# Kernel optimization log

Hardware: AMD Instinct MI355X
Metric: run time of the kernel (lower is better)

Reference implementation:

```python
import jax, jax.numpy as jnp
import numpy as np

K = 3          # pred_ks
EMB_SCALE = 1.0


def _unfold(x, k):
    # torch nn.Unfold(kernel=k, padding=(k-1)//2, stride=1), channel-major (C, kh, kw)
    B, C, H, W = x.shape
    p = (k - 1) // 2
    xp = jnp.pad(x, ((0, 0), (0, 0), (p, p), (p, p)))
    pats = jnp.stack([xp[:, :, i:i + H, j:j + W] for i in range(k) for j in range(k)], axis=2)
    return pats.reshape(B, C * k * k, H, W)


def _gs2d_nearest(x, grid):
    # F.grid_sample(mode='nearest', padding_mode='zeros', align_corners=False)
    B, C, H, W = x.shape
    ix = jnp.round((grid[..., 0] + 1.0) * W / 2.0 - 0.5)
    iy = jnp.round((grid[..., 1] + 1.0) * H / 2.0 - 0.5)
    valid = (ix >= 0) & (ix <= W - 1) & (iy >= 0) & (iy <= H - 1)
    ixc = jnp.clip(ix, 0, W - 1).astype(jnp.int32)
    iyc = jnp.clip(iy, 0, H - 1).astype(jnp.int32)

    def samp(img, yy, xx, vv):
        return jnp.where(vv[None], img[:, yy, xx], 0.0)

    return jax.vmap(samp)(x, iyc, ixc, valid)


def _gs3d_trilinear(vol, coords):
    # F.grid_sample 3D, mode='bilinear', padding_mode='zeros', align_corners=False
    # vol [C,D,H,W]; coords [N,3] with (x->W, y->H, z->D)
    C, D, H, W = vol.shape
    x = (coords[:, 0] + 1.0) * W / 2.0 - 0.5
    y = (coords[:, 1] + 1.0) * H / 2.0 - 0.5
    z = (coords[:, 2] + 1.0) * D / 2.0 - 0.5
    x0, y0, z0 = jnp.floor(x), jnp.floor(y), jnp.floor(z)
    vol_f = vol.reshape(C, D * H * W)
    out = jnp.zeros((C, coords.shape[0]), vol.dtype)
    for dz in (0.0, 1.0):
        for dy in (0.0, 1.0):
            for dx in (0.0, 1.0):
                xi, yi, zi = x0 + dx, y0 + dy, z0 + dz
                wgt = (1.0 - jnp.abs(x - xi)) * (1.0 - jnp.abs(y - yi)) * (1.0 - jnp.abs(z - zi))
                valid = (xi >= 0) & (xi <= W - 1) & (yi >= 0) & (yi <= H - 1) & (zi >= 0) & (zi <= D - 1)
                idx = (jnp.clip(zi, 0, D - 1) * (H * W) + jnp.clip(yi, 0, H - 1) * W
                       + jnp.clip(xi, 0, W - 1)).astype(jnp.int32)
                out = out + vol_f[:, idx] * jnp.where(valid, wgt, 0.0)[None]
    return out


def setup_inputs() -> dict:
    key = jax.random.key(0)
    ks = jax.random.split(key, 7)
    B, H, W = 4, 64, 64
    NV, VL, NS = 16, 4, 16
    f = jnp.float32
    grid1 = jax.random.uniform(ks[0], (B, H, W, 2), f, -1.0, 1.0)
    grid2 = jax.random.uniform(ks[1], (B, H, W, 2), f, -1.0, 1.0)
    theta = jax.random.uniform(ks[2], (B,), f, -np.pi, np.pi)
    lgn = jax.random.normal(ks[3], (B, NV * VL, H, W), f)
    coefx = jax.random.uniform(ks[4], (NV, VL, VL, NS), f, -0.1, 0.1)
    coefy = jax.random.uniform(ks[5], (NV, VL, VL, NS), f, -0.1, 0.1)
    coefr = jax.random.uniform(ks[6], (NV, VL, VL, NS), f, -0.1, 0.1)
    return {"grid1": grid1, "grid2": grid2, "theta": theta, "lgn": lgn,
            "coefx": coefx, "coefy": coefy, "coefr": coefr}


def reference(grid1, grid2, theta, lgn, coefx, coefy, coefr):
    B, C, H, W = lgn.shape
    NV, VL, _, NS = coefx.shape
    KS2 = K * K
    # unfold + rearrange to [b, c*ks2, h, w]
    uf_lgn = _unfold(lgn, K)
    uf_g1 = _unfold(jnp.transpose(grid1, (0, 3, 1, 2)), K)
    # nearest-neighbor warps by grid2
    uf_lgn_t = _gs2d_nearest(uf_lgn, grid2)
    uf_g1_t = _gs2d_nearest(uf_g1, grid2)
    g1 = uf_g1_t.reshape(B, 2, KS2, H, W)
    g2 = jnp.transpose(grid2, (0, 3, 1, 2))[:, :, None]          # [b,2,1,h,w]
    d = (g2 - g1) * EMB_SCALE                                    # [b,2,ks2,h,w]
    d = jnp.transpose(d, (0, 2, 3, 4, 1)).reshape(B, KS2 * H * W, 2)
    th = jnp.broadcast_to((theta / np.pi)[:, None, None], (B, KS2 * H * W, 1))
    coords = jnp.concatenate([d, th], axis=-1).reshape(B * KS2 * H * W, 3)
    # separable coefficient volume: x along H-axis, y along D-axis, r along W-axis
    w1 = jnp.einsum('ijkn,iklm->ijlmn', coefx, coefy)            # (nv,vl,vl,D,H)
    coef = jnp.einsum('ijkmn,iklo->ijlmno', w1, coefr)           # (nv,vl,vl,D,H,W)
    vol = coef.reshape(NV * VL * VL, NS, NS, NS)
    samples = _gs3d_trilinear(vol, coords)                       # [nv*vl*vl, b*ks2*h*w]
    coef_ = samples.reshape(NV, VL, VL, B, KS2, H * W)
    coef_ = jnp.transpose(coef_, (3, 5, 4, 0, 1, 2))             # [b,hw,ks2,nv,vl,vl]
    lgn_ = uf_lgn_t.reshape(B, NV, VL, KS2, H * W)
    lgn_ = jnp.transpose(lgn_, (0, 4, 3, 1, 2))                  # [b,hw,ks2,nv,vl]
    pred = jnp.einsum('bsknij,bsknj->bsni', coef_, lgn_)         # matmul + sum over ks2
    return jnp.transpose(pred, (0, 2, 3, 1)).reshape(B, NV * VL, H, W)
```

## Files before the change

kernel.cpp:

```cpp
#include <hip/hip_runtime.h>
#include <hip/hip_fp16.h>
#include <cstdint>

#define BB   4
#define IH   64
#define IW   64
#define HWN  4096
#define NVN  16
#define NSN  16


#define EWS_OFF  (BB*HWN*64*2)
#define CWS_OFF  (EWS_OFF + BB*NVN*NSN*16*2)

struct __align__(16) H2x4 { __half2 h[4]; };
struct __align__(8)  H2x2 { __half2 a, b; };

__global__ __launch_bounds__(256) void prep_kernel(
    const float* __restrict__ lgn, const float* __restrict__ theta,
    const float* __restrict__ coefx, const float* __restrict__ coefy,
    const float* __restrict__ coefr, char* __restrict__ ws)
{
    const int blk = blockIdx.x, t = threadIdx.x;
    if (blk < 256) {
        __shared__ float tile[64][65];
        const int b = blk >> 6, hwbase = (blk & 63) << 6;
        const float* src = lgn + (size_t)b * (64 * HWN);
        const int r0 = t >> 6, x0 = t & 63;
        #pragma unroll
        for (int i = 0; i < 16; ++i) {
            const int c = r0 + i * 4;
            tile[c][x0] = src[c * HWN + hwbase + x0];
        }
        __syncthreads();
        __half2* dst = (__half2*)ws + (size_t)b * (HWN * 32);
        const int cp = t & 31, hwo = t >> 5;
        #pragma unroll
        for (int it = 0; it < 8; ++it) {
            const int hw = hwo + it * 8;
            dst[(hwbase + hw) * 32 + cp] =
                __floats2half2_rn(tile[2 * cp][hw], tile[2 * cp + 1][hw]);
        }
    } else if (blk < 288) {
        const int p  = (blk - 256) * 256 + t;
        const int b  = p >> 11, nv = (p >> 7) & 15, n = (p >> 3) & 15, q = p & 7;
        const float th  = theta[b] * 0.31830988618379067154f;
        const float zf  = (th + 1.0f) * 8.0f - 0.5f;
        const float zfl = floorf(zf);
        const float fz  = zf - zfl;
        const int   m0  = (int)zfl;
        const float wz0 = (m0 >= 0 && m0 <= 15) ? (1.0f - fz) : 0.0f;
        const float wz1 = (m0 + 1 >= 0 && m0 + 1 <= 15) ? fz : 0.0f;
        const int   m0c = min(max(m0, 0), 15), m1c = min(max(m0 + 1, 0), 15);
        float ev[2];
        #pragma unroll
        for (int s = 0; s < 2; ++s) {
            const int idx = 2 * q + s, j = idx >> 2, k2 = idx & 3;
            float e = 0.0f;
            #pragma unroll
            for (int k1 = 0; k1 < 4; ++k1) {
                const float a  = coefx[nv * 256 + (j * 4 + k1) * 16 + n];
                const float bm = wz0 * coefy[nv * 256 + (k1 * 4 + k2) * 16 + m0c]
                               + wz1 * coefy[nv * 256 + (k1 * 4 + k2) * 16 + m1c];
                e += a * bm;
            }
            ev[s] = e;
        }
        ((__half2*)(ws + EWS_OFF))[p] = __floats2half2_rn(ev[0], ev[1]);
    } else {
        const int p = (blk - 288) * 256 + t;
        if (p < 2048) {
            const int nv = p >> 7, o = (p >> 3) & 15, q = p & 7;
            const float c0 = coefr[nv * 256 + (2 * q + 0) * 16 + o];
            const float c1 = coefr[nv * 256 + (2 * q + 1) * 16 + o];
            ((__half2*)(ws + CWS_OFF))[p] = __floats2half2_rn(c0, c1);
        }
    }
}

__global__ __launch_bounds__(256) void seprot_kernel(
    const float* __restrict__ grid1,
    const float* __restrict__ grid2,
    const char*  __restrict__ ws,
    float* __restrict__ out)
{
    __shared__ H2x4 sC[768];
    __shared__ H2x4 sE[768];

    const int t   = threadIdx.x;
    const int blk = blockIdx.x;
    const int b      = blk >> 8;
    const int hwbase = (blk & 255) << 4;
    const int pg = t >> 4;
    const int nv = t & 15;
    const int hw = hwbase + pg;

    {
        const H2x4* Cw = (const H2x4*)(ws + CWS_OFF);
        const H2x4* Ew = (const H2x4*)(ws + EWS_OFF) + b * 512;
        #pragma unroll
        for (int k = 0; k < 2; ++k) {
            const int i  = t + k * 256;
            const int wnv = i >> 5, wo = (i >> 1) & 15, wu = i & 1;
            const int du = wo * 48 + wnv * 3 + wu;
            sC[du] = Cw[i];
            sE[du] = Ew[i];
        }
    }
    __syncthreads();

    const float2 g2  = ((const float2*)grid2)[b * HWN + hw];
    const float  sxf = rintf((g2.x + 1.0f) * (0.5f * IW) - 0.5f);
    const float  syf = rintf((g2.y + 1.0f) * (0.5f * IH) - 0.5f);
    const bool valid = (sxf >= 0.0f) && (sxf <= (float)(IW - 1)) &&
                       (syf >= 0.0f) && (syf <= (float)(IH - 1));

    const int obase = (b * 64 + nv * 4) * HWN + hw;

    if (!valid) {
        #pragma unroll
        for (int j = 0; j < 4; ++j) out[obase + j * HWN] = 0.0f;
        return;
    }

    const int sx = (int)sxf, sy = (int)syf;
    const __half2 zero2 = __floats2half2_rn(0.0f, 0.0f);
    float acc[4] = {0.0f, 0.0f, 0.0f, 0.0f};

    #pragma unroll
    for (int tap = 0; tap < 9; ++tap) {
        const int di = tap / 3 - 1, dj = tap % 3 - 1;
        const int ty = sy + di, tx = sx + dj;
        const bool inb = ((unsigned)ty < (unsigned)IH) && ((unsigned)tx < (unsigned)IW);
        const int pix = min(max(ty, 0), IH - 1) * IW + min(max(tx, 0), IW - 1);

        H2x2 lgu = ((const H2x2*)ws)[(b * HWN + pix) * 16 + nv];
        __half2 lg01 = inb ? lgu.a : zero2;
        __half2 lg23 = inb ? lgu.b : zero2;

        const float2 g1 = ((const float2*)grid1)[b * HWN + pix];
        const float dxc = g2.x - g1.x;
        const float dyc = g2.y - g1.y;

        const float xf  = (dxc + 1.0f) * (0.5f * NSN) - 0.5f;
        const float xfl = floorf(xf);
        const float fx  = xf - xfl;
        const int   o0  = (int)xfl;
        const float wx0 = (o0 >= 0 && o0 <= NSN - 1) ? (1.0f - fx) : 0.0f;
        const float wx1 = (o0 + 1 >= 0 && o0 + 1 <= NSN - 1) ? fx : 0.0f;
        const int   o0c = min(max(o0, 0), NSN - 1);
        const int   o1c = min(max(o0 + 1, 0), NSN - 1);

        const float yf  = (dyc + 1.0f) * (0.5f * NSN) - 0.5f;
        const float yfl = floorf(yf);
        const float fy  = yf - yfl;
        const int   n0  = (int)yfl;
        const float wy0 = (n0 >= 0 && n0 <= NSN - 1) ? (1.0f - fy) : 0.0f;
        const float wy1 = (n0 + 1 >= 0 && n0 + 1 <= NSN - 1) ? fy : 0.0f;
        const int   n0c = min(max(n0, 0), NSN - 1);
        const int   n1c = min(max(n0 + 1, 0), NSN - 1);

        const __half2 wx0h = __floats2half2_rn(wx0, wx0);
        const __half2 wx1h = __floats2half2_rn(wx1, wx1);
        const __half2 wy0h = __floats2half2_rn(wy0, wy0);
        const __half2 wy1h = __floats2half2_rn(wy1, wy1);

        const H2x4 c0a = sC[o0c * 48 + nv * 3 + 0];
        const H2x4 c0b = sC[o0c * 48 + nv * 3 + 1];
        const H2x4 c1a = sC[o1c * 48 + nv * 3 + 0];
        const H2x4 c1b = sC[o1c * 48 + nv * 3 + 1];
        __half2 bl[8];
        #pragma unroll
        for (int k = 0; k < 4; ++k) {
            bl[k]     = __hfma2(c0a.h[k], wx0h, __hmul2(c1a.h[k], wx1h));
            bl[4 + k] = __hfma2(c0b.h[k], wx0h, __hmul2(c1b.h[k], wx1h));
        }
        float vf[4];
        #pragma unroll
        for (int k2 = 0; k2 < 4; ++k2) {
            const __half2 sv = __hfma2(bl[2 * k2 + 1], lg23,
                                       __hmul2(bl[2 * k2], lg01));
            vf[k2] = __low2float(sv) + __high2float(sv);
        }
        const __half2 v01 = __floats2half2_rn(vf[0], vf[1]);
        const __half2 v23 = __floats2half2_rn(vf[2], vf[3]);

        const H2x4 e0a = sE[n0c * 48 + nv * 3 + 0];
        const H2x4 e0b = sE[n0c * 48 + nv * 3 + 1];
        const H2x4 e1a = sE[n1c * 48 + nv * 3 + 0];
        const H2x4 e1b = sE[n1c * 48 + nv * 3 + 1];
        __half2 eb[8];
        #pragma unroll
        for (int k = 0; k < 4; ++k) {
            eb[k]     = __hfma2(e0a.h[k], wy0h, __hmul2(e1a.h[k], wy1h));
            eb[4 + k] = __hfma2(e0b.h[k], wy0h, __hmul2(e1b.h[k], wy1h));
        }
        #pragma unroll
        for (int j = 0; j < 4; ++j) {
            const __half2 sa = __hfma2(eb[2 * j + 1], v23,
                                       __hmul2(eb[2 * j], v01));
            acc[j] += __low2float(sa) + __high2float(sa);
        }
    }

    #pragma unroll
    for (int j = 0; j < 4; ++j)
        out[obase + j * HWN] = acc[j];
}

extern "C" void kernel_launch(void* const* d_in, const int* in_sizes, int n_in,
                              void* d_out, int out_size, void* d_ws, size_t ws_size,
                              hipStream_t stream) {
    const float* grid1 = (const float*)d_in[0];
    const float* grid2 = (const float*)d_in[1];
    const float* theta = (const float*)d_in[2];
    const float* lgn   = (const float*)d_in[3];
    const float* coefx = (const float*)d_in[4];
    const float* coefy = (const float*)d_in[5];
    const float* coefr = (const float*)d_in[6];
    float*       outp  = (float*)d_out;
    char*        ws    = (char*)d_ws;

    hipLaunchKernelGGL(prep_kernel, dim3(296), dim3(256), 0, stream,
                       lgn, theta, coefx, coefy, coefr, ws);

    hipLaunchKernelGGL(seprot_kernel, dim3(BB * 256), dim3(256), 0, stream,
                       grid1, grid2, ws, outp);
}
```

Measured before the change: 82.68 us.

## Coalesce output stores via shared transpose, vectorize prep loads, pad LDS tables

The main kernel now stages each thread's four accumulators in shared memory and transposes them, so global writes run contiguously along hw instead of striding across channels. The early return for invalid pixels is replaced by a guarded block, so every thread reaches the barrier and writes zeros through the same path. The coefficient tables in LDS get a row stride of 49 to reduce bank conflicts. The prep kernel's lgn transpose uses float4 loads and smaller tiles across twice as many blocks. The extra barrier and shared buffer may cost some occupancy.

```diff
diff --git a/kernel.cpp b/kernel.cpp
--- a/kernel.cpp
+++ b/kernel.cpp
@@ -22,27 +22,33 @@
     const float* __restrict__ coefr, char* __restrict__ ws)
 {
     const int blk = blockIdx.x, t = threadIdx.x;
-    if (blk < 256) {
-        __shared__ float tile[64][65];
-        const int b = blk >> 6, hwbase = (blk & 63) << 6;
-        const float* src = lgn + (size_t)b * (64 * HWN);
-        const int r0 = t >> 6, x0 = t & 63;
-        #pragma unroll
-        for (int i = 0; i < 16; ++i) {
-            const int c = r0 + i * 4;
-            tile[c][x0] = src[c * HWN + hwbase + x0];
+    if (blk < 512) {
+        __shared__ float tile[64][33];
+        const int b      = blk >> 7;
+        const int hwbase = (blk & 127) << 5;
+        const float* src = lgn + (size_t)b * (64 * HWN) + hwbase;
+        const int x4 = t & 7;
+        const int c0 = t >> 3;
+        #pragma unroll
+        for (int i = 0; i < 2; ++i) {
+            const int c = c0 + i * 32;
+            const float4 v = *(const float4*)&src[c * HWN + x4 * 4];
+            tile[c][x4 * 4 + 0] = v.x;
+            tile[c][x4 * 4 + 1] = v.y;
+            tile[c][x4 * 4 + 2] = v.z;
+            tile[c][x4 * 4 + 3] = v.w;
         }
         __syncthreads();
-        __half2* dst = (__half2*)ws + (size_t)b * (HWN * 32);
-        const int cp = t & 31, hwo = t >> 5;
-        #pragma unroll
-        for (int it = 0; it < 8; ++it) {
-            const int hw = hwo + it * 8;
-            dst[(hwbase + hw) * 32 + cp] =
+        __half2* dst = (__half2*)ws + (size_t)b * (HWN * 32) + (size_t)hwbase * 32;
+        const int cp = t & 31, hw0 = t >> 5;
+        #pragma unroll
+        for (int i = 0; i < 4; ++i) {
+            const int hw = hw0 + i * 8;
+            dst[hw * 32 + cp] =
                 __floats2half2_rn(tile[2 * cp][hw], tile[2 * cp + 1][hw]);
         }
-    } else if (blk < 288) {
-        const int p  = (blk - 256) * 256 + t;
+    } else if (blk < 544) {
+        const int p  = (blk - 512) * 256 + t;
         const int b  = p >> 11, nv = (p >> 7) & 15, n = (p >> 3) & 15, q = p & 7;
         const float th  = theta[b] * 0.31830988618379067154f;
         const float zf  = (th + 1.0f) * 8.0f - 0.5f;
@@ -68,7 +74,7 @@
         }
         ((__half2*)(ws + EWS_OFF))[p] = __floats2half2_rn(ev[0], ev[1]);
     } else {
-        const int p = (blk - 288) * 256 + t;
+        const int p = (blk - 544) * 256 + t;
         if (p < 2048) {
             const int nv = p >> 7, o = (p >> 3) & 15, q = p & 7;
             const float c0 = coefr[nv * 256 + (2 * q + 0) * 16 + o];
@@ -84,8 +90,9 @@
     const char*  __restrict__ ws,
     float* __restrict__ out)
 {
-    __shared__ H2x4 sC[768];
-    __shared__ H2x4 sE[768];
+    __shared__ H2x4 sC[16 * 49];
+    __shared__ H2x4 sE[16 * 49];
+    __shared__ float sOut[16][17][4];
 
     const int t   = threadIdx.x;
     const int blk = blockIdx.x;
@@ -100,9 +107,9 @@
         const H2x4* Ew = (const H2x4*)(ws + EWS_OFF) + b * 512;
         #pragma unroll
         for (int k = 0; k < 2; ++k) {
-            const int i  = t + k * 256;
+            const int i   = t + k * 256;
             const int wnv = i >> 5, wo = (i >> 1) & 15, wu = i & 1;
-            const int du = wo * 48 + wnv * 3 + wu;
+            const int du  = wo * 49 + wnv * 3 + wu;
             sC[du] = Cw[i];
             sE[du] = Ew[i];
         }
@@ -115,97 +122,97 @@
     const bool valid = (sxf >= 0.0f) && (sxf <= (float)(IW - 1)) &&
                        (syf >= 0.0f) && (syf <= (float)(IH - 1));
 
-    const int obase = (b * 64 + nv * 4) * HWN + hw;
-
-    if (!valid) {
-        #pragma unroll
-        for (int j = 0; j < 4; ++j) out[obase + j * HWN] = 0.0f;
-        return;
-    }
-
-    const int sx = (int)sxf, sy = (int)syf;
-    const __half2 zero2 = __floats2half2_rn(0.0f, 0.0f);
     float acc[4] = {0.0f, 0.0f, 0.0f, 0.0f};
 
-    #pragma unroll
-    for (int tap = 0; tap < 9; ++tap) {
-        const int di = tap / 3 - 1, dj = tap % 3 - 1;
-        const int ty = sy + di, tx = sx + dj;
-        const bool inb = ((unsigned)ty < (unsigned)IH) && ((unsigned)tx < (unsigned)IW);
-        const int pix = min(max(ty, 0), IH - 1) * IW + min(max(tx, 0), IW - 1);
-
-        H2x2 lgu = ((const H2x2*)ws)[(b * HWN + pix) * 16 + nv];
-        __half2 lg01 = inb ? lgu.a : zero2;
-        __half2 lg23 = inb ? lgu.b : zero2;
-
-        const float2 g1 = ((const float2*)grid1)[b * HWN + pix];
-        const float dxc = g2.x - g1.x;
-        const float dyc = g2.y - g1.y;
-
-        const float xf  = (dxc + 1.0f) * (0.5f * NSN) - 0.5f;
-        const float xfl = floorf(xf);
-        const float fx  = xf - xfl;
-        const int   o0  = (int)xfl;
-        const float wx0 = (o0 >= 0 && o0 <= NSN - 1) ? (1.0f - fx) : 0.0f;
-        const float wx1 = (o0 + 1 >= 0 && o0 + 1 <= NSN - 1) ? fx : 0.0f;
-        const int   o0c = min(max(o0, 0), NSN - 1);
-        const int   o1c = min(max(o0 + 1, 0), NSN - 1);
-
-        const float yf  = (dyc + 1.0f) * (0.5f * NSN) - 0.5f;
-        const float yfl = floorf(yf);
-        const float fy  = yf - yfl;
-        const int   n0  = (int)yfl;
-        const float wy0 = (n0 >= 0 && n0 <= NSN - 1) ? (1.0f - fy) : 0.0f;
-        const float wy1 = (n0 + 1 >= 0 && n0 + 1 <= NSN - 1) ? fy : 0.0f;
-        const int   n0c = min(max(n0, 0), NSN - 1);
-        const int   n1c = min(max(n0 + 1, 0), NSN - 1);
-
-        const __half2 wx0h = __floats2half2_rn(wx0, wx0);
-        const __half2 wx1h = __floats2half2_rn(wx1, wx1);
-        const __half2 wy0h = __floats2half2_rn(wy0, wy0);
-        const __half2 wy1h = __floats2half2_rn(wy1, wy1);
-
-        const H2x4 c0a = sC[o0c * 48 + nv * 3 + 0];
-        const H2x4 c0b = sC[o0c * 48 + nv * 3 + 1];
-        const H2x4 c1a = sC[o1c * 48 + nv * 3 + 0];
-        const H2x4 c1b = sC[o1c * 48 + nv * 3 + 1];
-        __half2 bl[8];
-        #pragma unroll
-        for (int k = 0; k < 4; ++k) {
-            bl[k]     = __hfma2(c0a.h[k], wx0h, __hmul2(c1a.h[k], wx1h));
-            bl[4 + k] = __hfma2(c0b.h[k], wx0h, __hmul2(c1b.h[k], wx1h));
-        }
-        float vf[4];
-        #pragma unroll
-        for (int k2 = 0; k2 < 4; ++k2) {
-            const __half2 sv = __hfma2(bl[2 * k2 + 1], lg23,
-                                       __hmul2(bl[2 * k2], lg01));
-            vf[k2] = __low2float(sv) + __high2float(sv);
-        }
-        const __half2 v01 = __floats2half2_rn(vf[0], vf[1]);
-        const __half2 v23 = __floats2half2_rn(vf[2], vf[3]);
-
-        const H2x4 e0a = sE[n0c * 48 + nv * 3 + 0];
-        const H2x4 e0b = sE[n0c * 48 + nv * 3 + 1];
-        const H2x4 e1a = sE[n1c * 48 + nv * 3 + 0];
-        const H2x4 e1b = sE[n1c * 48 + nv * 3 + 1];
-        __half2 eb[8];
-        #pragma unroll
-        for (int k = 0; k < 4; ++k) {
-            eb[k]     = __hfma2(e0a.h[k], wy0h, __hmul2(e1a.h[k], wy1h));
-            eb[4 + k] = __hfma2(e0b.h[k], wy0h, __hmul2(e1b.h[k], wy1h));
-        }
-        #pragma unroll
-        for (int j = 0; j < 4; ++j) {
-            const __half2 sa = __hfma2(eb[2 * j + 1], v23,
-                                       __hmul2(eb[2 * j], v01));
-            acc[j] += __low2float(sa) + __high2float(sa);
-        }
-    }
-
-    #pragma unroll
-    for (int j = 0; j < 4; ++j)
-        out[obase + j * HWN] = acc[j];
+    if (valid) {
+        const int sx = (int)sxf, sy = (int)syf;
+        const __half2 zero2 = __floats2half2_rn(0.0f, 0.0f);
+
+        #pragma unroll
+        for (int tap = 0; tap < 9; ++tap) {
+            const int di = tap / 3 - 1, dj = tap % 3 - 1;
+            const int ty = sy + di, tx = sx + dj;
+            const bool inb = ((unsigned)ty < (unsigned)IH) && ((unsigned)tx < (unsigned)IW);
+            const int pix = min(max(ty, 0), IH - 1) * IW + min(max(tx, 0), IW - 1);
+
+            H2x2 lgu = ((const H2x2*)ws)[(b * HWN + pix) * 16 + nv];
+            __half2 lg01 = inb ? lgu.a : zero2;
+            __half2 lg23 = inb ? lgu.b : zero2;
+
+            const float2 g1 = ((const float2*)grid1)[b * HWN + pix];
+            const float dxc = g2.x - g1.x;
+            const float dyc = g2.y - g1.y;
+
+            const float xf  = (dxc + 1.0f) * (0.5f * NSN) - 0.5f;
+            const float xfl = floorf(xf);
+            const float fx  = xf - xfl;
+            const int   o0  = (int)xfl;
+            const float wx0 = (o0 >= 0 && o0 <= NSN - 1) ? (1.0f - fx) : 0.0f;
+            const float wx1 = (o0 + 1 >= 0 && o0 + 1 <= NSN - 1) ? fx : 0.0f;
+            const int   o0c = min(max(o0, 0), NSN - 1);
+            const int   o1c = min(max(o0 + 1, 0), NSN - 1);
+
+            const float yf  = (dyc + 1.0f) * (0.5f * NSN) - 0.5f;
+            const float yfl = floorf(yf);
+            const float fy  = yf - yfl;
+            const int   n0  = (int)yfl;
+            const float wy0 = (n0 >= 0 && n0 <= NSN - 1) ? (1.0f - fy) : 0.0f;
+            const float wy1 = (n0 + 1 >= 0 && n0 + 1 <= NSN - 1) ? fy : 0.0f;
+            const int   n0c = min(max(n0, 0), NSN - 1);
+            const int   n1c = min(max(n0 + 1, 0), NSN - 1);
+
+            const __half2 wx0h = __floats2half2_rn(wx0, wx0);
+            const __half2 wx1h = __floats2half2_rn(wx1, wx1);
+            const __half2 wy0h = __floats2half2_rn(wy0, wy0);
+            const __half2 wy1h = __floats2half2_rn(wy1, wy1);
+
+            const H2x4 c0a = sC[o0c * 49 + nv * 3 + 0];
+            const H2x4 c0b = sC[o0c * 49 + nv * 3 + 1];
+            const H2x4 c1a = sC[o1c * 49 + nv * 3 + 0];
+            const H2x4 c1b = sC[o1c * 49 + nv * 3 + 1];
+            __half2 bl[8];
+            #pragma unroll
+            for (int k = 0; k < 4; ++k) {
+                bl[k]     = __hfma2(c0a.h[k], wx0h, __hmul2(c1a.h[k], wx1h));
+                bl[4 + k] = __hfma2(c0b.h[k], wx0h, __hmul2(c1b.h[k], wx1h));
+            }
+            float vf[4];
+            #pragma unroll
+            for (int k2 = 0; k2 < 4; ++k2) {
+                const __half2 sv = __hfma2(bl[2 * k2 + 1], lg23,
+                                           __hmul2(bl[2 * k2], lg01));
+                vf[k2] = __low2float(sv) + __high2float(sv);
+            }
+            const __half2 v01 = __floats2half2_rn(vf[0], vf[1]);
+            const __half2 v23 = __floats2half2_rn(vf[2], vf[3]);
+
+            const H2x4 e0a = sE[n0c * 49 + nv * 3 + 0];
+            const H2x4 e0b = sE[n0c * 49 + nv * 3 + 1];
+            const H2x4 e1a = sE[n1c * 49 + nv * 3 + 0];
+            const H2x4 e1b = sE[n1c * 49 + nv * 3 + 1];
+            __half2 eb[8];
+            #pragma unroll
+            for (int k = 0; k < 4; ++k) {
+                eb[k]     = __hfma2(e0a.h[k], wy0h, __hmul2(e1a.h[k], wy1h));
+                eb[4 + k] = __hfma2(e0b.h[k], wy0h, __hmul2(e1b.h[k], wy1h));
+            }
+            #pragma unroll
+            for (int j = 0; j < 4; ++j) {
+                const __half2 sa = __hfma2(eb[2 * j + 1], v23,
+                                           __hmul2(eb[2 * j], v01));
+                acc[j] += __low2float(sa) + __high2float(sa);
+            }
+        }
+    }
+
+    *(float4*)&sOut[pg][nv][0] = make_float4(acc[0], acc[1], acc[2], acc[3]);
+    __syncthreads();
+    {
+        const int nv2 = t >> 4, pg2 = t & 15;
+        #pragma unroll
+        for (int j = 0; j < 4; ++j)
+            out[(b * 64 + nv2 * 4 + j) * HWN + hwbase + pg2] = sOut[pg2][nv2][j];
+    }
 }
 
 extern "C" void kernel_launch(void* const* d_in, const int* in_sizes, int n_in,
@@ -221,7 +228,7 @@
     float*       outp  = (float*)d_out;
     char*        ws    = (char*)d_ws;
 
-    hipLaunchKernelGGL(prep_kernel, dim3(296), dim3(256), 0, stream,
+    hipLaunchKernelGGL(prep_kernel, dim3(552), dim3(256), 0, stream,
                        lgn, theta, coefx, coefy, coefr, ws);
 
     hipLaunchKernelGGL(seprot_kernel, dim3(BB * 256), dim3(256), 0, stream,
```

Measured after the change: 82.61 us, median of 2. Within noise of the previous version (-0.1%).
